# Performance work log

Measured on AMD Instinct MI355X. Metric: run time of the kernel, lower is better.

The kernel has to match this reference:

```python
import jax, jax.numpy as jnp
import numpy as np

DIM = 768
HEADS = 12
DIM_HEAD = 64
INNER = HEADS * DIM_HEAD  # 768
SCALE = DIM_HEAD ** -0.5
LN_EPS = 1e-5


def setup_inputs() -> dict:
    key = jax.random.key(0)
    ks = jax.random.split(key, 6)
    B, N = 2, 1024
    x = jax.random.normal(ks[0], (B, N, DIM), dtype=jnp.float32)
    ln_g = jnp.ones((DIM,), jnp.float32)
    ln_b = jnp.zeros((DIM,), jnp.float32)
    # torch nn.Linear weights are [out, in]
    w_qkv = jax.random.normal(ks[1], (3 * INNER, DIM), jnp.float32) * (DIM ** -0.5)
    w_out = jax.random.normal(ks[2], (DIM, INNER), jnp.float32) * (INNER ** -0.5)
    b_out = jnp.zeros((DIM,), jnp.float32)
    theta = jax.random.normal(ks[3], (HEADS, HEADS), jnp.float32)
    # xavier_uniform for 12x12
    lim = float(np.sqrt(6.0 / (HEADS + HEADS)))
    gnn_w = jax.random.uniform(ks[4], (HEADS, HEADS), jnp.float32, -lim, lim)
    return {"x": x, "ln_g": ln_g, "ln_b": ln_b, "w_qkv": w_qkv,
            "w_out": w_out, "b_out": b_out, "theta": theta, "gnn_w": gnn_w}


def _dc_crd(attn, theta, gnn_w):
    # attn: [B, H, N, N] treated as image with H=12 channels
    B, H, N, _ = attn.shape
    w = attn.mean(axis=(-2, -1))  # adaptive_avg_pool2d -> [B, H]
    diff = w[:, :, None] - w[:, None, :]  # [B, H, H]
    # abs(1 - exp(-d)/(1+exp(-d))) - 1 == abs(1 - sigmoid(-d)) - 1
    T_w = jnp.abs(1.0 - jax.nn.sigmoid(-diff)) - 1.0
    adj = (T_w + jnp.swapaxes(T_w, -1, -2)) * 0.5 * theta  # [B, H, H]
    attn_flat = attn.reshape(B, H, N * N)
    support = jnp.einsum('ij,bjm->bim', gnn_w, attn_flat)  # W @ features
    out = jax.nn.relu(jnp.einsum('bij,bjm->bim', adj, support))  # spmm(adj, support)
    return out.reshape(B, H, N, N)


def reference(x, ln_g, ln_b, w_qkv, w_out, b_out, theta, gnn_w):
    B, N, D = x.shape
    mu = x.mean(-1, keepdims=True)
    var = x.var(-1, keepdims=True)
    xn = (x - mu) * jax.lax.rsqrt(var + LN_EPS) * ln_g + ln_b
    qkv = xn @ w_qkv.T  # [B, N, 3*INNER]
    q, k, v = jnp.split(qkv, 3, axis=-1)
    def heads(t):
        return t.reshape(B, N, HEADS, DIM_HEAD).transpose(0, 2, 1, 3)
    q, k, v = heads(q), heads(k), heads(v)  # [B, H, N, d]
    dots = jnp.einsum('bhnd,bhmd->bhnm', q, k) * SCALE
    attn = jax.nn.softmax(dots, axis=-1)
    H = _dc_crd(attn, theta, gnn_w)
    out = jnp.einsum('bhnm,bhmd->bhnd', attn + H, v)
    out = out.transpose(0, 2, 1, 3).reshape(B, N, INNER)
    return out @ w_out.T + b_out
```

## Files before the change

### kernel.cpp

```cpp
#include <hip/hip_runtime.h>
#include <hip/hip_bf16.h>
#include <stdint.h>

#define NB 2
#define SEQ 1024
#define DMODEL 768
#define NH 12
#define DH 64
#define SCALE 0.125f
#define NCH 4

typedef __hip_bfloat16 bf16;
typedef __attribute__((ext_vector_type(8))) short short8;
typedef __attribute__((ext_vector_type(4))) float f32x4;

__device__ __forceinline__ float b2f(bf16 x){ return __bfloat162float(x); }
__device__ __forceinline__ bf16 f2b(float x){ return __float2bfloat16(x); }
__device__ __forceinline__ short f2bs(float x){
  bf16 h = __float2bfloat16(x); return *reinterpret_cast<short*>(&h);
}
__device__ __forceinline__ float s2f(short u){
  return __uint_as_float(((unsigned)(unsigned short)u) << 16);
}

__global__ __launch_bounds__(256) void cvt_kernel(const float* __restrict__ src,
                                                  bf16* __restrict__ dst, int n){
  int i = blockIdx.x*256 + threadIdx.x;
  if (i < n) dst[i] = f2b(src[i]);
}

__global__ __launch_bounds__(256) void ln_kernel(const float* __restrict__ x,
                                                 const float* __restrict__ g,
                                                 const float* __restrict__ bta,
                                                 bf16* __restrict__ xn){
  int row = blockIdx.x; int t = threadIdx.x;
  const float* xr = x + (size_t)row*DMODEL;
  float v0[3]; float s = 0.f, s2 = 0.f;
  #pragma unroll
  for (int i=0;i<3;i++){ float val = xr[t+256*i]; v0[i]=val; s+=val; s2+=val*val; }
  __shared__ float sb[256], s2b[256];
  sb[t]=s; s2b[t]=s2; __syncthreads();
  for (int off=128; off>0; off>>=1){
    if (t<off){ sb[t]+=sb[t+off]; s2b[t]+=s2b[t+off]; }
    __syncthreads();
  }
  float mean = sb[0]*(1.f/DMODEL);
  float var  = s2b[0]*(1.f/DMODEL) - mean*mean;
  float rstd = rsqrtf(var + 1e-5f);
  #pragma unroll
  for (int i=0;i<3;i++){
    int c = t+256*i;
    xn[(size_t)row*DMODEL + c] = f2b((v0[i]-mean)*rstd*g[c] + bta[c]);
  }
}

__global__ __launch_bounds__(256) void prep_kernel(const float* __restrict__ theta,
                                                   const float* __restrict__ gnn,
                                                   float* __restrict__ Mm,
                                                   float* __restrict__ l){
  int bx = blockIdx.x, t = threadIdx.x;
  if (bx == 0){
    if (t < 144){
      int i = t/12, kx = t%12;
      float sacc = 0.f;
      for (int j=0;j<12;j++) sacc += (-0.5f)*theta[i*12+j] * gnn[j*12+kx];
      Mm[t] = sacc;
    }
  } else {
    l[(bx-1)*256 + t] = 0.f;
  }
}

__global__ __launch_bounds__(256) void gemm_qkv(const bf16* __restrict__ A,
                                                const bf16* __restrict__ W,
                                                bf16* __restrict__ q,
                                                bf16* __restrict__ k,
                                                bf16* __restrict__ vt){
  __shared__ bf16 As[128*32];
  __shared__ bf16 Bs[128*32];
  int n0 = blockIdx.x*128, m0 = blockIdx.y*128;
  int t = threadIdx.x, w = t>>6, lane = t&63;
  int ln16 = lane&15, q8 = (lane>>4)*8;
  int wm = w>>1, wn = w&1;
  f32x4 acc[4][4] = {};
  for (int k0=0; k0<768; k0+=32){
    __syncthreads();
    #pragma unroll
    for (int i=0;i<2;i++){
      int cc = t + i*256;
      int r = cc>>2, ko = (cc&3)*8;
      *(short8*)&As[r*32+ko] = *(const short8*)&A[(size_t)(m0+r)*768 + k0+ko];
      *(short8*)&Bs[r*32+ko] = *(const short8*)&W[(size_t)(n0+r)*768 + k0+ko];
    }
    __syncthreads();
    short8 af[4], bfr[4];
    #pragma unroll
    for (int mi=0;mi<4;mi++) af[mi]  = *(const short8*)&As[(wm*64+mi*16+ln16)*32 + q8];
    #pragma unroll
    for (int ni=0;ni<4;ni++) bfr[ni] = *(const short8*)&Bs[(wn*64+ni*16+ln16)*32 + q8];
    #pragma unroll
    for (int mi=0;mi<4;mi++)
      #pragma unroll
      for (int ni=0;ni<4;ni++)
        acc[mi][ni] = __builtin_amdgcn_mfma_f32_16x16x32_bf16(af[mi], bfr[ni], acc[mi][ni], 0, 0, 0);
  }
  int quad4 = (lane>>4)*4;
  #pragma unroll
  for (int mi=0;mi<4;mi++){
    #pragma unroll
    for (int ni=0;ni<4;ni++){
      int cg = n0 + wn*64 + ni*16 + ln16;
      int which = cg/768; int rem = cg - which*768;
      int h = rem>>6, dd = rem&63;
      #pragma unroll
      for (int r=0;r<4;r++){
        int m = m0 + wm*64 + mi*16 + quad4 + r;
        int bb = m>>10, n = m&1023;
        float val = acc[mi][ni][r];
        if (which==0)      q [((size_t)(bb*NH+h)*SEQ + n)*DH + dd] = f2b(val*SCALE);
        else if (which==1) k [((size_t)(bb*NH+h)*SEQ + n)*DH + dd] = f2b(val);
        else               vt[((size_t)(bb*NH+h)*DH + dd)*SEQ + n] = f2b(val);
      }
    }
  }
}

__global__ __launch_bounds__(768) void attn_sums(const bf16* __restrict__ q,
                                                 const bf16* __restrict__ k,
                                                 float* __restrict__ l){
  int b = blockIdx.z, ch = blockIdx.y; int r0 = blockIdx.x*16;
  int t = threadIdx.x; int h = t>>6; int lane = t&63;
  int ln16 = lane&15, quad = lane>>4; int q8 = quad*8, quad4 = quad*4;
  const bf16* qrow = q + ((size_t)(b*NH+h)*SEQ + r0 + ln16)*DH;
  short8 aq0 = *(const short8*)(qrow + q8);
  short8 aq1 = *(const short8*)(qrow + 32 + q8);
  const bf16* kB = k + ((size_t)(b*NH+h)*SEQ)*DH;
  float ls[4] = {0.f,0.f,0.f,0.f};
  for (int i=0;i<16;i++){
    int c0 = ch*256 + i*16;
    const bf16* krow = kB + (size_t)(c0 + ln16)*DH;
    short8 bk0 = *(const short8*)(krow + q8);
    short8 bk1 = *(const short8*)(krow + 32 + q8);
    f32x4 a = {0.f,0.f,0.f,0.f};
    a = __builtin_amdgcn_mfma_f32_16x16x32_bf16(aq0, bk0, a, 0, 0, 0);
    a = __builtin_amdgcn_mfma_f32_16x16x32_bf16(aq1, bk1, a, 0, 0, 0);
    #pragma unroll
    for (int r=0;r<4;r++) ls[r] += __expf(a[r]);
  }
  #pragma unroll
  for (int msk=1; msk<16; msk<<=1){
    #pragma unroll
    for (int r=0;r<4;r++) ls[r] += __shfl_xor(ls[r], msk);
  }
  if (ln16 == 0){
    #pragma unroll
    for (int r=0;r<4;r++)
      atomicAdd(&l[((size_t)(b*NH+h))*SEQ + r0 + quad4 + r], ls[r]);
  }
}

__global__ __launch_bounds__(768) void attn_main(const bf16* __restrict__ q,
                                                 const bf16* __restrict__ k,
                                                 const bf16* __restrict__ vt,
                                                 const float* __restrict__ Mm,
                                                 const float* __restrict__ l,
                                                 float* __restrict__ opart){
  __shared__ bf16 attT[2][NH][16][40];
  __shared__ float Ms[144];
  int b = blockIdx.z, ch = blockIdx.y; int r0 = blockIdx.x*16;
  int t = threadIdx.x; int h = t>>6; int lane = t&63;
  int ln16 = lane&15, quad = lane>>4; int q8 = quad*8, quad4 = quad*4;
  const bf16* kB = k  + ((size_t)(b*NH+h)*SEQ)*DH;
  const bf16* vB = vt + ((size_t)(b*NH+h)*DH)*SEQ;

  if (t < 144) Ms[t] = Mm[t];

  const bf16* qrow = q + ((size_t)(b*NH+h)*SEQ + r0 + ln16)*DH;
  short8 aq0 = *(const short8*)(qrow + q8);
  short8 aq1 = *(const short8*)(qrow + 32 + q8);

  float inv_l[4];
  #pragma unroll
  for (int r=0;r<4;r++) inv_l[r] = 1.0f / l[((size_t)(b*NH+h))*SEQ + r0 + quad4 + r];

  f32x4 oacc[4] = {};
  for (int it=0; it<8; it++){
    int c0 = ch*256 + it*32;
    int buf = it&1;
    #pragma unroll
    for (int half=0; half<2; half++){
      const bf16* krow = kB + (size_t)(c0 + half*16 + ln16)*DH;
      short8 bk0 = *(const short8*)(krow + q8);
      short8 bk1 = *(const short8*)(krow + 32 + q8);
      f32x4 a = {0.f,0.f,0.f,0.f};
      a = __builtin_amdgcn_mfma_f32_16x16x32_bf16(aq0, bk0, a, 0, 0, 0);
      a = __builtin_amdgcn_mfma_f32_16x16x32_bf16(aq1, bk1, a, 0, 0, 0);
      #pragma unroll
      for (int r=0;r<4;r++)
        attT[buf][h][quad4+r][half*16 + ln16] = f2b(__expf(a[r])*inv_l[r]);
    }
    __syncthreads();
    float sm[8] = {0.f,0.f,0.f,0.f,0.f,0.f,0.f,0.f};
    #pragma unroll
    for (int j=0;j<12;j++){
      short8 u = *(const short8*)&attT[buf][j][ln16][q8];
      float m = Ms[h*12+j];
      #pragma unroll
      for (int e=0;e<8;e++) sm[e] += m*s2f(u[e]);
    }
    short8 uh = *(const short8*)&attT[buf][h][ln16][q8];
    short8 afrag;
    #pragma unroll
    for (int e=0;e<8;e++) afrag[e] = f2bs(s2f(uh[e]) + fmaxf(sm[e], 0.f));
    #pragma unroll
    for (int ni=0; ni<4; ni++){
      short8 bv = *(const short8*)&vB[(size_t)(ni*16 + ln16)*SEQ + c0 + q8];
      oacc[ni] = __builtin_amdgcn_mfma_f32_16x16x32_bf16(afrag, bv, oacc[ni], 0, 0, 0);
    }
  }
  float* dst = opart + ((size_t)ch*NB*SEQ + (size_t)b*SEQ)*DMODEL;
  #pragma unroll
  for (int ni=0; ni<4; ni++)
    #pragma unroll
    for (int r=0; r<4; r++){
      int n = r0 + quad4 + r;
      dst[(size_t)n*DMODEL + h*DH + ni*16 + ln16] = oacc[ni][r];
    }
}

__global__ __launch_bounds__(256) void reduce_kernel(const float* __restrict__ opart,
                                                     bf16* __restrict__ aout){
  const size_t TOT = (size_t)NB*SEQ*DMODEL;
  size_t i = ((size_t)blockIdx.x*256 + threadIdx.x)*4;
  float4 s = *(const float4*)&opart[i];
  #pragma unroll
  for (int c=1;c<NCH;c++){
    float4 p = *(const float4*)&opart[c*TOT + i];
    s.x += p.x; s.y += p.y; s.z += p.z; s.w += p.w;
  }
  aout[i+0]=f2b(s.x); aout[i+1]=f2b(s.y); aout[i+2]=f2b(s.z); aout[i+3]=f2b(s.w);
}

__global__ __launch_bounds__(256) void gemm_out(const bf16* __restrict__ A,
                                                const bf16* __restrict__ W,
                                                const float* __restrict__ bias,
                                                float* __restrict__ out){
  __shared__ bf16 As[128*32];
  __shared__ bf16 Bs[128*32];
  int n0 = blockIdx.x*128, m0 = blockIdx.y*128;
  int t = threadIdx.x, w = t>>6, lane = t&63;
  int ln16 = lane&15, q8 = (lane>>4)*8;
  int wm = w>>1, wn = w&1;
  f32x4 acc[4][4] = {};
  for (int k0=0; k0<768; k0+=32){
    __syncthreads();
    #pragma unroll
    for (int i=0;i<2;i++){
      int cc = t + i*256;
      int r = cc>>2, ko = (cc&3)*8;
      *(short8*)&As[r*32+ko] = *(const short8*)&A[(size_t)(m0+r)*768 + k0+ko];
      *(short8*)&Bs[r*32+ko] = *(const short8*)&W[(size_t)(n0+r)*768 + k0+ko];
    }
    __syncthreads();
    short8 af[4], bfr[4];
    #pragma unroll
    for (int mi=0;mi<4;mi++) af[mi]  = *(const short8*)&As[(wm*64+mi*16+ln16)*32 + q8];
    #pragma unroll
    for (int ni=0;ni<4;ni++) bfr[ni] = *(const short8*)&Bs[(wn*64+ni*16+ln16)*32 + q8];
    #pragma unroll
    for (int mi=0;mi<4;mi++)
      #pragma unroll
      for (int ni=0;ni<4;ni++)
        acc[mi][ni] = __builtin_amdgcn_mfma_f32_16x16x32_bf16(af[mi], bfr[ni], acc[mi][ni], 0, 0, 0);
  }
  int quad4 = (lane>>4)*4;
  #pragma unroll
  for (int mi=0;mi<4;mi++)
    #pragma unroll
    for (int ni=0;ni<4;ni++){
      int cg = n0 + wn*64 + ni*16 + ln16;
      #pragma unroll
      for (int r=0;r<4;r++){
        int m = m0 + wm*64 + mi*16 + quad4 + r;
        out[(size_t)m*768 + cg] = acc[mi][ni][r] + bias[cg];
      }
    }
}

extern "C" void kernel_launch(void* const* d_in, const int* in_sizes, int n_in,
                              void* d_out, int out_size, void* d_ws, size_t ws_size,
                              hipStream_t stream){
  const float* x     = (const float*)d_in[0];
  const float* ln_g  = (const float*)d_in[1];
  const float* ln_b  = (const float*)d_in[2];
  const float* w_qkv = (const float*)d_in[3];
  const float* w_out = (const float*)d_in[4];
  const float* b_out = (const float*)d_in[5];
  const float* theta = (const float*)d_in[6];
  const float* gnn   = (const float*)d_in[7];
  float* out = (float*)d_out;

  char* p = (char*)d_ws;
  bf16* xnb   = (bf16*)p; p += (size_t)2048*768*2;
  bf16* wqkvb = (bf16*)p; p += (size_t)2304*768*2;
  bf16* woutb = (bf16*)p; p += (size_t)768*768*2;
  bf16* qb    = (bf16*)p; p += (size_t)NB*NH*SEQ*DH*2;
  bf16* kb    = (bf16*)p; p += (size_t)NB*NH*SEQ*DH*2;
  bf16* vtb   = (bf16*)p; p += (size_t)NB*NH*SEQ*DH*2;
  bf16* aoutb = (bf16*)p; p += (size_t)2048*768*2;
  float* Mm   = (float*)p; p += 256*4;
  float* lsum = (float*)p; p += (size_t)NB*NH*SEQ*4;
  float* opart= (float*)p;

  cvt_kernel<<<dim3((2304*768+255)/256), dim3(256), 0, stream>>>(w_qkv, wqkvb, 2304*768);
  cvt_kernel<<<dim3((768*768+255)/256),  dim3(256), 0, stream>>>(w_out, woutb, 768*768);
  ln_kernel<<<dim3(NB*SEQ), dim3(256), 0, stream>>>(x, ln_g, ln_b, xnb);
  prep_kernel<<<dim3(97), dim3(256), 0, stream>>>(theta, gnn, Mm, lsum);
  gemm_qkv<<<dim3(18, 16), dim3(256), 0, stream>>>(xnb, wqkvb, qb, kb, vtb);
  attn_sums<<<dim3(64, NCH, NB), dim3(768), 0, stream>>>(qb, kb, lsum);
  attn_main<<<dim3(64, NCH, NB), dim3(768), 0, stream>>>(qb, kb, vtb, Mm, lsum, opart);
  reduce_kernel<<<dim3((NB*SEQ*DMODEL/4+255)/256), dim3(256), 0, stream>>>(opart, aoutb);
  gemm_out<<<dim3(6, 16), dim3(256), 0, stream>>>(aoutb, woutb, b_out, out);
}
```

Baseline: 214.8 us.

## Use direct global-to-LDS loads in GEMMs and fp32 attention staging

Both GEMM kernels now load tiles with the global_load_lds builtin, writing straight into shared memory instead of going through registers. The LDS base per wave is computed as w*64+i*256 times 8, which relies on the hardware placing each lane's 16 bytes consecutively. In attn_main the shared attention tile becomes fp32 (padded to 44), so the 12-head mixing reads float4s and skips bf16 round-tripping, and the V fragment loads are hoisted above the barrier so they overlap with it. attn_sums gets an unroll-4 pragma. The fp32 tile roughly doubles shared-memory use, and the direct-to-LDS addressing is correct only if the builtin's per-lane placement matches the As/Bs layout that readers expect.

Measured after the change: 220.9 us. +2.8%, slower.

```diff
diff --git a/kernel.cpp b/kernel.cpp
--- a/kernel.cpp
+++ b/kernel.cpp
@@ -21,6 +21,12 @@
 }
 __device__ __forceinline__ float s2f(short u){
   return __uint_as_float(((unsigned)(unsigned short)u) << 16);
+}
+
+__device__ __forceinline__ void gl_lds16(const bf16* g, bf16* l){
+  __builtin_amdgcn_global_load_lds(
+      (const __attribute__((address_space(1))) void*)g,
+      (__attribute__((address_space(3))) void*)l, 16, 0, 0);
 }
 
 __global__ __launch_bounds__(256) void cvt_kernel(const float* __restrict__ src,
@@ -89,8 +95,8 @@
     for (int i=0;i<2;i++){
       int cc = t + i*256;
       int r = cc>>2, ko = (cc&3)*8;
-      *(short8*)&As[r*32+ko] = *(const short8*)&A[(size_t)(m0+r)*768 + k0+ko];
-      *(short8*)&Bs[r*32+ko] = *(const short8*)&W[(size_t)(n0+r)*768 + k0+ko];
+      gl_lds16(&A[(size_t)(m0+r)*768 + k0+ko], &As[(size_t)(w*64 + i*256)*8]);
+      gl_lds16(&W[(size_t)(n0+r)*768 + k0+ko], &Bs[(size_t)(w*64 + i*256)*8]);
     }
     __syncthreads();
     short8 af[4], bfr[4];
@@ -136,6 +142,7 @@
   short8 aq1 = *(const short8*)(qrow + 32 + q8);
   const bf16* kB = k + ((size_t)(b*NH+h)*SEQ)*DH;
   float ls[4] = {0.f,0.f,0.f,0.f};
+  #pragma unroll 4
   for (int i=0;i<16;i++){
     int c0 = ch*256 + i*16;
     const bf16* krow = kB + (size_t)(c0 + ln16)*DH;
@@ -165,7 +172,7 @@
                                                  const float* __restrict__ Mm,
                                                  const float* __restrict__ l,
                                                  float* __restrict__ opart){
-  __shared__ bf16 attT[2][NH][16][40];
+  __shared__ float attT[2][NH][16][44];
   __shared__ float Ms[144];
   int b = blockIdx.z, ch = blockIdx.y; int r0 = blockIdx.x*16;
   int t = threadIdx.x; int h = t>>6; int lane = t&63;
@@ -197,26 +204,34 @@
       a = __builtin_amdgcn_mfma_f32_16x16x32_bf16(aq1, bk1, a, 0, 0, 0);
       #pragma unroll
       for (int r=0;r<4;r++)
-        attT[buf][h][quad4+r][half*16 + ln16] = f2b(__expf(a[r])*inv_l[r]);
-    }
+        attT[buf][h][quad4+r][half*16 + ln16] = __expf(a[r])*inv_l[r];
+    }
+    short8 bv[4];
+    #pragma unroll
+    for (int ni=0; ni<4; ni++)
+      bv[ni] = *(const short8*)&vB[(size_t)(ni*16 + ln16)*SEQ + c0 + q8];
     __syncthreads();
     float sm[8] = {0.f,0.f,0.f,0.f,0.f,0.f,0.f,0.f};
     #pragma unroll
     for (int j=0;j<12;j++){
-      short8 u = *(const short8*)&attT[buf][j][ln16][q8];
+      const float* row = &attT[buf][j][ln16][q8];
+      float4 u0 = *(const float4*)row;
+      float4 u1 = *(const float4*)(row+4);
       float m = Ms[h*12+j];
-      #pragma unroll
-      for (int e=0;e<8;e++) sm[e] += m*s2f(u[e]);
-    }
-    short8 uh = *(const short8*)&attT[buf][h][ln16][q8];
+      sm[0] += m*u0.x; sm[1] += m*u0.y; sm[2] += m*u0.z; sm[3] += m*u0.w;
+      sm[4] += m*u1.x; sm[5] += m*u1.y; sm[6] += m*u1.z; sm[7] += m*u1.w;
+    }
+    const float* hrow = &attT[buf][h][ln16][q8];
+    float4 h0 = *(const float4*)hrow;
+    float4 h1 = *(const float4*)(hrow+4);
     short8 afrag;
-    #pragma unroll
-    for (int e=0;e<8;e++) afrag[e] = f2bs(s2f(uh[e]) + fmaxf(sm[e], 0.f));
-    #pragma unroll
-    for (int ni=0; ni<4; ni++){
-      short8 bv = *(const short8*)&vB[(size_t)(ni*16 + ln16)*SEQ + c0 + q8];
-      oacc[ni] = __builtin_amdgcn_mfma_f32_16x16x32_bf16(afrag, bv, oacc[ni], 0, 0, 0);
-    }
+    afrag[0] = f2bs(h0.x + fmaxf(sm[0],0.f)); afrag[1] = f2bs(h0.y + fmaxf(sm[1],0.f));
+    afrag[2] = f2bs(h0.z + fmaxf(sm[2],0.f)); afrag[3] = f2bs(h0.w + fmaxf(sm[3],0.f));
+    afrag[4] = f2bs(h1.x + fmaxf(sm[4],0.f)); afrag[5] = f2bs(h1.y + fmaxf(sm[5],0.f));
+    afrag[6] = f2bs(h1.z + fmaxf(sm[6],0.f)); afrag[7] = f2bs(h1.w + fmaxf(sm[7],0.f));
+    #pragma unroll
+    for (int ni=0; ni<4; ni++)
+      oacc[ni] = __builtin_amdgcn_mfma_f32_16x16x32_bf16(afrag, bv[ni], oacc[ni], 0, 0, 0);
   }
   float* dst = opart + ((size_t)ch*NB*SEQ + (size_t)b*SEQ)*DMODEL;
   #pragma unroll
@@ -258,8 +273,8 @@
     for (int i=0;i<2;i++){
       int cc = t + i*256;
       int r = cc>>2, ko = (cc&3)*8;
-      *(short8*)&As[r*32+ko] = *(const short8*)&A[(size_t)(m0+r)*768 + k0+ko];
-      *(short8*)&Bs[r*32+ko] = *(const short8*)&W[(size_t)(n0+r)*768 + k0+ko];
+      gl_lds16(&A[(size_t)(m0+r)*768 + k0+ko], &As[(size_t)(w*64 + i*256)*8]);
+      gl_lds16(&W[(size_t)(n0+r)*768 + k0+ko], &Bs[(size_t)(w*64 + i*256)*8]);
     }
     __syncthreads();
     short8 af[4], bfr[4];
```

## Materialize exp scores in global memory, fuse prep kernels, use direct LDS loads

Applied to the files above, without the earlier changes.

The prep kernels (layernorm, weight conversion, M matrix and l zeroing) are merged into one launch. attn_exp now writes bf16 exp(QK) values for every head to a 48 MB global buffer alongside the row sums. attn_main reads those values back instead of recomputing QK and exp, folds 1/l into the per-head mixing coefficients, and splits the key dimension into 8 chunks. The GEMMs switch to global_load_lds direct-to-LDS copies. This trades recomputed QK work and LDS staging for heavy extra global memory traffic and a larger partial-sum reduction.

Result: slower. 265.2 us (+23.4%).

```diff
diff --git a/kernel.cpp b/kernel.cpp
--- a/kernel.cpp
+++ b/kernel.cpp
@@ -8,13 +8,13 @@
 #define NH 12
 #define DH 64
 #define SCALE 0.125f
-#define NCH 4
+#define NCHE 4
+#define NCHM 8
 
 typedef __hip_bfloat16 bf16;
 typedef __attribute__((ext_vector_type(8))) short short8;
 typedef __attribute__((ext_vector_type(4))) float f32x4;
 
-__device__ __forceinline__ float b2f(bf16 x){ return __bfloat162float(x); }
 __device__ __forceinline__ bf16 f2b(float x){ return __float2bfloat16(x); }
 __device__ __forceinline__ short f2bs(float x){
   bf16 h = __float2bfloat16(x); return *reinterpret_cast<short*>(&h);
@@ -23,51 +23,59 @@
   return __uint_as_float(((unsigned)(unsigned short)u) << 16);
 }
 
-__global__ __launch_bounds__(256) void cvt_kernel(const float* __restrict__ src,
-                                                  bf16* __restrict__ dst, int n){
-  int i = blockIdx.x*256 + threadIdx.x;
-  if (i < n) dst[i] = f2b(src[i]);
-}
-
-__global__ __launch_bounds__(256) void ln_kernel(const float* __restrict__ x,
-                                                 const float* __restrict__ g,
-                                                 const float* __restrict__ bta,
-                                                 bf16* __restrict__ xn){
-  int row = blockIdx.x; int t = threadIdx.x;
-  const float* xr = x + (size_t)row*DMODEL;
-  float v0[3]; float s = 0.f, s2 = 0.f;
-  #pragma unroll
-  for (int i=0;i<3;i++){ float val = xr[t+256*i]; v0[i]=val; s+=val; s2+=val*val; }
-  __shared__ float sb[256], s2b[256];
-  sb[t]=s; s2b[t]=s2; __syncthreads();
-  for (int off=128; off>0; off>>=1){
-    if (t<off){ sb[t]+=sb[t+off]; s2b[t]+=s2b[t+off]; }
-    __syncthreads();
-  }
-  float mean = sb[0]*(1.f/DMODEL);
-  float var  = s2b[0]*(1.f/DMODEL) - mean*mean;
-  float rstd = rsqrtf(var + 1e-5f);
-  #pragma unroll
-  for (int i=0;i<3;i++){
-    int c = t+256*i;
-    xn[(size_t)row*DMODEL + c] = f2b((v0[i]-mean)*rstd*g[c] + bta[c]);
-  }
-}
-
-__global__ __launch_bounds__(256) void prep_kernel(const float* __restrict__ theta,
-                                                   const float* __restrict__ gnn,
-                                                   float* __restrict__ Mm,
-                                                   float* __restrict__ l){
+__device__ __forceinline__ void gl_lds16(const bf16* g, bf16* l){
+  __builtin_amdgcn_global_load_lds(
+      (const __attribute__((address_space(1))) void*)g,
+      (__attribute__((address_space(3))) void*)l, 16, 0, 0);
+}
+
+__global__ __launch_bounds__(256) void prep_all(const float* __restrict__ x,
+                                                const float* __restrict__ g,
+                                                const float* __restrict__ bta,
+                                                const float* __restrict__ w1, int n1,
+                                                const float* __restrict__ w2, int n2,
+                                                const float* __restrict__ theta,
+                                                const float* __restrict__ gnn,
+                                                bf16* __restrict__ xn,
+                                                bf16* __restrict__ wb,
+                                                float* __restrict__ Mm,
+                                                float* __restrict__ l){
   int bx = blockIdx.x, t = threadIdx.x;
-  if (bx == 0){
-    if (t < 144){
-      int i = t/12, kx = t%12;
-      float sacc = 0.f;
-      for (int j=0;j<12;j++) sacc += (-0.5f)*theta[i*12+j] * gnn[j*12+kx];
-      Mm[t] = sacc;
-    }
+  if (bx < 2048){
+    const float* xr = x + (size_t)bx*DMODEL;
+    float v0[3]; float s = 0.f, s2 = 0.f;
+    #pragma unroll
+    for (int i=0;i<3;i++){ float val = xr[t+256*i]; v0[i]=val; s+=val; s2+=val*val; }
+    __shared__ float sb[256], s2b[256];
+    sb[t]=s; s2b[t]=s2; __syncthreads();
+    for (int off=128; off>0; off>>=1){
+      if (t<off){ sb[t]+=sb[t+off]; s2b[t]+=s2b[t+off]; }
+      __syncthreads();
+    }
+    float mean = sb[0]*(1.f/DMODEL);
+    float var  = s2b[0]*(1.f/DMODEL) - mean*mean;
+    float rstd = rsqrtf(var + 1e-5f);
+    #pragma unroll
+    for (int i=0;i<3;i++){
+      int c = t+256*i;
+      xn[(size_t)bx*DMODEL + c] = f2b((v0[i]-mean)*rstd*g[c] + bta[c]);
+    }
+  } else if (bx < 2048+9216){
+    int i = (bx-2048)*256 + t;
+    if (i < n1) wb[i] = f2b(w1[i]);
+    else if (i < n1+n2) wb[i] = f2b(w2[i-n1]);
   } else {
-    l[(bx-1)*256 + t] = 0.f;
+    int sub = bx - (2048+9216);
+    if (sub == 0){
+      if (t < 144){
+        int i = t/12, kx = t%12;
+        float sacc = 0.f;
+        for (int j=0;j<12;j++) sacc += (-0.5f)*theta[i*12+j] * gnn[j*12+kx];
+        Mm[t] = sacc;
+      }
+    } else {
+      l[(sub-1)*256 + t] = 0.f;
+    }
   }
 }
 
@@ -89,8 +97,8 @@
     for (int i=0;i<2;i++){
       int cc = t + i*256;
       int r = cc>>2, ko = (cc&3)*8;
-      *(short8*)&As[r*32+ko] = *(const short8*)&A[(size_t)(m0+r)*768 + k0+ko];
-      *(short8*)&Bs[r*32+ko] = *(const short8*)&W[(size_t)(n0+r)*768 + k0+ko];
+      gl_lds16(&A[(size_t)(m0+r)*768 + k0+ko], &As[(size_t)(w*64 + i*256)*8]);
+      gl_lds16(&W[(size_t)(n0+r)*768 + k0+ko], &Bs[(size_t)(w*64 + i*256)*8]);
     }
     __syncthreads();
     short8 af[4], bfr[4];
@@ -125,17 +133,22 @@
   }
 }
 
-__global__ __launch_bounds__(768) void attn_sums(const bf16* __restrict__ q,
-                                                 const bf16* __restrict__ k,
-                                                 float* __restrict__ l){
-  int b = blockIdx.z, ch = blockIdx.y; int r0 = blockIdx.x*16;
-  int t = threadIdx.x; int h = t>>6; int lane = t&63;
+__global__ __launch_bounds__(256) void attn_exp(const bf16* __restrict__ q,
+                                                const bf16* __restrict__ k,
+                                                float* __restrict__ l,
+                                                bf16* __restrict__ eg){
+  int strip = blockIdx.x, ch = blockIdx.y;
+  int b = blockIdx.z/3, hg = blockIdx.z%3;
+  int t = threadIdx.x; int h = hg*4 + (t>>6); int lane = t&63;
   int ln16 = lane&15, quad = lane>>4; int q8 = quad*8, quad4 = quad*4;
+  int r0 = strip*16;
   const bf16* qrow = q + ((size_t)(b*NH+h)*SEQ + r0 + ln16)*DH;
   short8 aq0 = *(const short8*)(qrow + q8);
   short8 aq1 = *(const short8*)(qrow + 32 + q8);
   const bf16* kB = k + ((size_t)(b*NH+h)*SEQ)*DH;
+  bf16* egh = eg + (((size_t)(b*NH+h))<<20);
   float ls[4] = {0.f,0.f,0.f,0.f};
+  #pragma unroll 4
   for (int i=0;i<16;i++){
     int c0 = ch*256 + i*16;
     const bf16* krow = kB + (size_t)(c0 + ln16)*DH;
@@ -145,7 +158,11 @@
     a = __builtin_amdgcn_mfma_f32_16x16x32_bf16(aq0, bk0, a, 0, 0, 0);
     a = __builtin_amdgcn_mfma_f32_16x16x32_bf16(aq1, bk1, a, 0, 0, 0);
     #pragma unroll
-    for (int r=0;r<4;r++) ls[r] += __expf(a[r]);
+    for (int r=0;r<4;r++){
+      float e = __expf(a[r]);
+      ls[r] += e;
+      egh[(size_t)(r0+quad4+r)*1024 + c0 + ln16] = f2b(e);
+    }
   }
   #pragma unroll
   for (int msk=1; msk<16; msk<<=1){
@@ -159,59 +176,42 @@
   }
 }
 
-__global__ __launch_bounds__(768) void attn_main(const bf16* __restrict__ q,
-                                                 const bf16* __restrict__ k,
+__global__ __launch_bounds__(768) void attn_main(const bf16* __restrict__ eg,
                                                  const bf16* __restrict__ vt,
                                                  const float* __restrict__ Mm,
                                                  const float* __restrict__ l,
                                                  float* __restrict__ opart){
-  __shared__ bf16 attT[2][NH][16][40];
-  __shared__ float Ms[144];
-  int b = blockIdx.z, ch = blockIdx.y; int r0 = blockIdx.x*16;
+  int strip = blockIdx.x, ch = blockIdx.y, b = blockIdx.z;
   int t = threadIdx.x; int h = t>>6; int lane = t&63;
   int ln16 = lane&15, quad = lane>>4; int q8 = quad*8, quad4 = quad*4;
-  const bf16* kB = k  + ((size_t)(b*NH+h)*SEQ)*DH;
-  const bf16* vB = vt + ((size_t)(b*NH+h)*DH)*SEQ;
-
-  if (t < 144) Ms[t] = Mm[t];
-
-  const bf16* qrow = q + ((size_t)(b*NH+h)*SEQ + r0 + ln16)*DH;
-  short8 aq0 = *(const short8*)(qrow + q8);
-  short8 aq1 = *(const short8*)(qrow + 32 + q8);
-
-  float inv_l[4];
-  #pragma unroll
-  for (int r=0;r<4;r++) inv_l[r] = 1.0f / l[((size_t)(b*NH+h))*SEQ + r0 + quad4 + r];
+  int r0 = strip*16;
+  const bf16* vB  = vt + ((size_t)(b*NH+h)*DH)*SEQ;
+  const bf16* egb = eg + (((size_t)b*NH)<<20);
+  const size_t rowoff = (size_t)(r0 + ln16)*1024;
+
+  float Mp[12];
+  #pragma unroll
+  for (int j=0;j<12;j++){
+    float lj = l[((size_t)(b*NH+j))*SEQ + r0 + ln16];
+    Mp[j] = Mm[h*12+j] / lj;
+  }
+  float ihl = 1.0f / l[((size_t)(b*NH+h))*SEQ + r0 + ln16];
 
   f32x4 oacc[4] = {};
-  for (int it=0; it<8; it++){
-    int c0 = ch*256 + it*32;
-    int buf = it&1;
-    #pragma unroll
-    for (int half=0; half<2; half++){
-      const bf16* krow = kB + (size_t)(c0 + half*16 + ln16)*DH;
-      short8 bk0 = *(const short8*)(krow + q8);
-      short8 bk1 = *(const short8*)(krow + 32 + q8);
-      f32x4 a = {0.f,0.f,0.f,0.f};
-      a = __builtin_amdgcn_mfma_f32_16x16x32_bf16(aq0, bk0, a, 0, 0, 0);
-      a = __builtin_amdgcn_mfma_f32_16x16x32_bf16(aq1, bk1, a, 0, 0, 0);
-      #pragma unroll
-      for (int r=0;r<4;r++)
-        attT[buf][h][quad4+r][half*16 + ln16] = f2b(__expf(a[r])*inv_l[r]);
-    }
-    __syncthreads();
+  for (int it=0; it<4; it++){
+    int c0 = ch*128 + it*32;
     float sm[8] = {0.f,0.f,0.f,0.f,0.f,0.f,0.f,0.f};
     #pragma unroll
     for (int j=0;j<12;j++){
-      short8 u = *(const short8*)&attT[buf][j][ln16][q8];
-      float m = Ms[h*12+j];
+      short8 u = *(const short8*)&egb[(((size_t)j)<<20) + rowoff + c0 + q8];
+      float m = Mp[j];
       #pragma unroll
       for (int e=0;e<8;e++) sm[e] += m*s2f(u[e]);
     }
-    short8 uh = *(const short8*)&attT[buf][h][ln16][q8];
+    short8 uh = *(const short8*)&egb[(((size_t)h)<<20) + rowoff + c0 + q8];
     short8 afrag;
     #pragma unroll
-    for (int e=0;e<8;e++) afrag[e] = f2bs(s2f(uh[e]) + fmaxf(sm[e], 0.f));
+    for (int e=0;e<8;e++) afrag[e] = f2bs(s2f(uh[e])*ihl + fmaxf(sm[e], 0.f));
     #pragma unroll
     for (int ni=0; ni<4; ni++){
       short8 bv = *(const short8*)&vB[(size_t)(ni*16 + ln16)*SEQ + c0 + q8];
@@ -234,7 +234,7 @@
   size_t i = ((size_t)blockIdx.x*256 + threadIdx.x)*4;
   float4 s = *(const float4*)&opart[i];
   #pragma unroll
-  for (int c=1;c<NCH;c++){
+  for (int c=1;c<NCHM;c++){
     float4 p = *(const float4*)&opart[c*TOT + i];
     s.x += p.x; s.y += p.y; s.z += p.z; s.w += p.w;
   }
@@ -258,8 +258,8 @@
     for (int i=0;i<2;i++){
       int cc = t + i*256;
       int r = cc>>2, ko = (cc&3)*8;
-      *(short8*)&As[r*32+ko] = *(const short8*)&A[(size_t)(m0+r)*768 + k0+ko];
-      *(short8*)&Bs[r*32+ko] = *(const short8*)&W[(size_t)(n0+r)*768 + k0+ko];
+      gl_lds16(&A[(size_t)(m0+r)*768 + k0+ko], &As[(size_t)(w*64 + i*256)*8]);
+      gl_lds16(&W[(size_t)(n0+r)*768 + k0+ko], &Bs[(size_t)(w*64 + i*256)*8]);
     }
     __syncthreads();
     short8 af[4], bfr[4];
@@ -310,15 +310,15 @@
   bf16* aoutb = (bf16*)p; p += (size_t)2048*768*2;
   float* Mm   = (float*)p; p += 256*4;
   float* lsum = (float*)p; p += (size_t)NB*NH*SEQ*4;
+  bf16* expg  = (bf16*)p; p += (size_t)NB*NH*SEQ*SEQ*2;
   float* opart= (float*)p;
 
-  cvt_kernel<<<dim3((2304*768+255)/256), dim3(256), 0, stream>>>(w_qkv, wqkvb, 2304*768);
-  cvt_kernel<<<dim3((768*768+255)/256),  dim3(256), 0, stream>>>(w_out, woutb, 768*768);
-  ln_kernel<<<dim3(NB*SEQ), dim3(256), 0, stream>>>(x, ln_g, ln_b, xnb);
-  prep_kernel<<<dim3(97), dim3(256), 0, stream>>>(theta, gnn, Mm, lsum);
+  const int N1 = 2304*768, N2 = 768*768;
+  prep_all<<<dim3(2048+9216+97), dim3(256), 0, stream>>>(
+      x, ln_g, ln_b, w_qkv, N1, w_out, N2, theta, gnn, xnb, wqkvb, Mm, lsum);
   gemm_qkv<<<dim3(18, 16), dim3(256), 0, stream>>>(xnb, wqkvb, qb, kb, vtb);
-  attn_sums<<<dim3(64, NCH, NB), dim3(768), 0, stream>>>(qb, kb, lsum);
-  attn_main<<<dim3(64, NCH, NB), dim3(768), 0, stream>>>(qb, kb, vtb, Mm, lsum, opart);
+  attn_exp<<<dim3(64, NCHE, NB*3), dim3(256), 0, stream>>>(qb, kb, lsum, expg);
+  attn_main<<<dim3(64, NCHM, NB), dim3(768), 0, stream>>>(expg, vtb, Mm, lsum, opart);
   reduce_kernel<<<dim3((NB*SEQ*DMODEL/4+255)/256), dim3(256), 0, stream>>>(opart, aoutb);
   gemm_out<<<dim3(6, 16), dim3(256), 0, stream>>>(aoutb, woutb, b_out, out);
 }
```

## Merge prep kernels, fold chunk reduce into out-GEMM K loop, use global_load_lds

Applied to the files above, without the earlier changes.

Merges LayerNorm, both weight conversions and the theta/gnn prep into one launch. The split-K partial outputs become bf16, and the reduce kernel is removed by having gemm_out run its K loop over all four chunks, which cuts launches and fp32 traffic at the cost of four times the MFMA work in the output GEMM. Both GEMMs now stage tiles with direct global-to-LDS loads, and attn_sums gets an unroll pragma. It risks bf16 rounding of the partial sums, and the LDS destination indexing under global_load_lds has to match the lane layout.

Measured after the change: 246.1 us. 14.6% more time.

```diff
diff --git a/kernel.cpp b/kernel.cpp
--- a/kernel.cpp
+++ b/kernel.cpp
@@ -14,7 +14,6 @@
 typedef __attribute__((ext_vector_type(8))) short short8;
 typedef __attribute__((ext_vector_type(4))) float f32x4;
 
-__device__ __forceinline__ float b2f(bf16 x){ return __bfloat162float(x); }
 __device__ __forceinline__ bf16 f2b(float x){ return __float2bfloat16(x); }
 __device__ __forceinline__ short f2bs(float x){
   bf16 h = __float2bfloat16(x); return *reinterpret_cast<short*>(&h);
@@ -23,51 +22,59 @@
   return __uint_as_float(((unsigned)(unsigned short)u) << 16);
 }
 
-__global__ __launch_bounds__(256) void cvt_kernel(const float* __restrict__ src,
-                                                  bf16* __restrict__ dst, int n){
-  int i = blockIdx.x*256 + threadIdx.x;
-  if (i < n) dst[i] = f2b(src[i]);
-}
-
-__global__ __launch_bounds__(256) void ln_kernel(const float* __restrict__ x,
-                                                 const float* __restrict__ g,
-                                                 const float* __restrict__ bta,
-                                                 bf16* __restrict__ xn){
-  int row = blockIdx.x; int t = threadIdx.x;
-  const float* xr = x + (size_t)row*DMODEL;
-  float v0[3]; float s = 0.f, s2 = 0.f;
-  #pragma unroll
-  for (int i=0;i<3;i++){ float val = xr[t+256*i]; v0[i]=val; s+=val; s2+=val*val; }
-  __shared__ float sb[256], s2b[256];
-  sb[t]=s; s2b[t]=s2; __syncthreads();
-  for (int off=128; off>0; off>>=1){
-    if (t<off){ sb[t]+=sb[t+off]; s2b[t]+=s2b[t+off]; }
-    __syncthreads();
-  }
-  float mean = sb[0]*(1.f/DMODEL);
-  float var  = s2b[0]*(1.f/DMODEL) - mean*mean;
-  float rstd = rsqrtf(var + 1e-5f);
-  #pragma unroll
-  for (int i=0;i<3;i++){
-    int c = t+256*i;
-    xn[(size_t)row*DMODEL + c] = f2b((v0[i]-mean)*rstd*g[c] + bta[c]);
-  }
-}
-
-__global__ __launch_bounds__(256) void prep_kernel(const float* __restrict__ theta,
-                                                   const float* __restrict__ gnn,
-                                                   float* __restrict__ Mm,
-                                                   float* __restrict__ l){
+__device__ __forceinline__ void gl_lds16(const bf16* g, bf16* l){
+  __builtin_amdgcn_global_load_lds(
+      (const __attribute__((address_space(1))) void*)g,
+      (__attribute__((address_space(3))) void*)l, 16, 0, 0);
+}
+
+__global__ __launch_bounds__(256) void prep_all(const float* __restrict__ x,
+                                                const float* __restrict__ g,
+                                                const float* __restrict__ bta,
+                                                const float* __restrict__ w1, int n1,
+                                                const float* __restrict__ w2, int n2,
+                                                const float* __restrict__ theta,
+                                                const float* __restrict__ gnn,
+                                                bf16* __restrict__ xn,
+                                                bf16* __restrict__ wb,
+                                                float* __restrict__ Mm,
+                                                float* __restrict__ l){
   int bx = blockIdx.x, t = threadIdx.x;
-  if (bx == 0){
-    if (t < 144){
-      int i = t/12, kx = t%12;
-      float sacc = 0.f;
-      for (int j=0;j<12;j++) sacc += (-0.5f)*theta[i*12+j] * gnn[j*12+kx];
-      Mm[t] = sacc;
-    }
+  if (bx < 2048){
+    const float* xr = x + (size_t)bx*DMODEL;
+    float v0[3]; float s = 0.f, s2 = 0.f;
+    #pragma unroll
+    for (int i=0;i<3;i++){ float val = xr[t+256*i]; v0[i]=val; s+=val; s2+=val*val; }
+    __shared__ float sb[256], s2b[256];
+    sb[t]=s; s2b[t]=s2; __syncthreads();
+    for (int off=128; off>0; off>>=1){
+      if (t<off){ sb[t]+=sb[t+off]; s2b[t]+=s2b[t+off]; }
+      __syncthreads();
+    }
+    float mean = sb[0]*(1.f/DMODEL);
+    float var  = s2b[0]*(1.f/DMODEL) - mean*mean;
+    float rstd = rsqrtf(var + 1e-5f);
+    #pragma unroll
+    for (int i=0;i<3;i++){
+      int c = t+256*i;
+      xn[(size_t)bx*DMODEL + c] = f2b((v0[i]-mean)*rstd*g[c] + bta[c]);
+    }
+  } else if (bx < 2048+9216){
+    int i = (bx-2048)*256 + t;
+    if (i < n1) wb[i] = f2b(w1[i]);
+    else if (i < n1+n2) wb[i] = f2b(w2[i-n1]);
   } else {
-    l[(bx-1)*256 + t] = 0.f;
+    int sub = bx - (2048+9216);
+    if (sub == 0){
+      if (t < 144){
+        int i = t/12, kx = t%12;
+        float sacc = 0.f;
+        for (int j=0;j<12;j++) sacc += (-0.5f)*theta[i*12+j] * gnn[j*12+kx];
+        Mm[t] = sacc;
+      }
+    } else {
+      l[(sub-1)*256 + t] = 0.f;
+    }
   }
 }
 
@@ -89,8 +96,8 @@
     for (int i=0;i<2;i++){
       int cc = t + i*256;
       int r = cc>>2, ko = (cc&3)*8;
-      *(short8*)&As[r*32+ko] = *(const short8*)&A[(size_t)(m0+r)*768 + k0+ko];
-      *(short8*)&Bs[r*32+ko] = *(const short8*)&W[(size_t)(n0+r)*768 + k0+ko];
+      gl_lds16(&A[(size_t)(m0+r)*768 + k0+ko], &As[(size_t)(w*64 + i*256)*8]);
+      gl_lds16(&W[(size_t)(n0+r)*768 + k0+ko], &Bs[(size_t)(w*64 + i*256)*8]);
     }
     __syncthreads();
     short8 af[4], bfr[4];
@@ -136,6 +143,7 @@
   short8 aq1 = *(const short8*)(qrow + 32 + q8);
   const bf16* kB = k + ((size_t)(b*NH+h)*SEQ)*DH;
   float ls[4] = {0.f,0.f,0.f,0.f};
+  #pragma unroll 4
   for (int i=0;i<16;i++){
     int c0 = ch*256 + i*16;
     const bf16* krow = kB + (size_t)(c0 + ln16)*DH;
@@ -164,7 +172,7 @@
                                                  const bf16* __restrict__ vt,
                                                  const float* __restrict__ Mm,
                                                  const float* __restrict__ l,
-                                                 float* __restrict__ opart){
+                                                 bf16* __restrict__ opart){
   __shared__ bf16 attT[2][NH][16][40];
   __shared__ float Ms[144];
   int b = blockIdx.z, ch = blockIdx.y; int r0 = blockIdx.x*16;
@@ -218,30 +226,17 @@
       oacc[ni] = __builtin_amdgcn_mfma_f32_16x16x32_bf16(afrag, bv, oacc[ni], 0, 0, 0);
     }
   }
-  float* dst = opart + ((size_t)ch*NB*SEQ + (size_t)b*SEQ)*DMODEL;
+  bf16* dst = opart + ((size_t)ch*NB*SEQ + (size_t)b*SEQ)*DMODEL;
   #pragma unroll
   for (int ni=0; ni<4; ni++)
     #pragma unroll
     for (int r=0; r<4; r++){
       int n = r0 + quad4 + r;
-      dst[(size_t)n*DMODEL + h*DH + ni*16 + ln16] = oacc[ni][r];
-    }
-}
-
-__global__ __launch_bounds__(256) void reduce_kernel(const float* __restrict__ opart,
-                                                     bf16* __restrict__ aout){
-  const size_t TOT = (size_t)NB*SEQ*DMODEL;
-  size_t i = ((size_t)blockIdx.x*256 + threadIdx.x)*4;
-  float4 s = *(const float4*)&opart[i];
-  #pragma unroll
-  for (int c=1;c<NCH;c++){
-    float4 p = *(const float4*)&opart[c*TOT + i];
-    s.x += p.x; s.y += p.y; s.z += p.z; s.w += p.w;
-  }
-  aout[i+0]=f2b(s.x); aout[i+1]=f2b(s.y); aout[i+2]=f2b(s.z); aout[i+3]=f2b(s.w);
-}
-
-__global__ __launch_bounds__(256) void gemm_out(const bf16* __restrict__ A,
+      dst[(size_t)n*DMODEL + h*DH + ni*16 + ln16] = f2b(oacc[ni][r]);
+    }
+}
+
+__global__ __launch_bounds__(256) void gemm_out(const bf16* __restrict__ opart,
                                                 const bf16* __restrict__ W,
                                                 const float* __restrict__ bias,
                                                 float* __restrict__ out){
@@ -252,14 +247,16 @@
   int ln16 = lane&15, q8 = (lane>>4)*8;
   int wm = w>>1, wn = w&1;
   f32x4 acc[4][4] = {};
-  for (int k0=0; k0<768; k0+=32){
+  for (int k0=0; k0<NCH*768; k0+=32){
+    int ch = k0/768, kk0 = k0 - ch*768;
+    const bf16* Aب = opart + (size_t)ch*NB*SEQ*DMODEL;
     __syncthreads();
     #pragma unroll
     for (int i=0;i<2;i++){
       int cc = t + i*256;
       int r = cc>>2, ko = (cc&3)*8;
-      *(short8*)&As[r*32+ko] = *(const short8*)&A[(size_t)(m0+r)*768 + k0+ko];
-      *(short8*)&Bs[r*32+ko] = *(const short8*)&W[(size_t)(n0+r)*768 + k0+ko];
+      gl_lds16(&Aب[(size_t)(m0+r)*768 + kk0+ko], &As[(size_t)(w*64 + i*256)*8]);
+      gl_lds16(&W[(size_t)(n0+r)*768 + kk0+ko], &Bs[(size_t)(w*64 + i*256)*8]);
     }
     __syncthreads();
     short8 af[4], bfr[4];
@@ -307,18 +304,15 @@
   bf16* qb    = (bf16*)p; p += (size_t)NB*NH*SEQ*DH*2;
   bf16* kb    = (bf16*)p; p += (size_t)NB*NH*SEQ*DH*2;
   bf16* vtb   = (bf16*)p; p += (size_t)NB*NH*SEQ*DH*2;
-  bf16* aoutb = (bf16*)p; p += (size_t)2048*768*2;
   float* Mm   = (float*)p; p += 256*4;
   float* lsum = (float*)p; p += (size_t)NB*NH*SEQ*4;
-  float* opart= (float*)p;
-
-  cvt_kernel<<<dim3((2304*768+255)/256), dim3(256), 0, stream>>>(w_qkv, wqkvb, 2304*768);
-  cvt_kernel<<<dim3((768*768+255)/256),  dim3(256), 0, stream>>>(w_out, woutb, 768*768);
-  ln_kernel<<<dim3(NB*SEQ), dim3(256), 0, stream>>>(x, ln_g, ln_b, xnb);
-  prep_kernel<<<dim3(97), dim3(256), 0, stream>>>(theta, gnn, Mm, lsum);
+  bf16* opart = (bf16*)p;
+
+  const int N1 = 2304*768, N2 = 768*768;
+  prep_all<<<dim3(2048+9216+97), dim3(256), 0, stream>>>(
+      x, ln_g, ln_b, w_qkv, N1, w_out, N2, theta, gnn, xnb, wqkvb, Mm, lsum);
   gemm_qkv<<<dim3(18, 16), dim3(256), 0, stream>>>(xnb, wqkvb, qb, kb, vtb);
   attn_sums<<<dim3(64, NCH, NB), dim3(768), 0, stream>>>(qb, kb, lsum);
   attn_main<<<dim3(64, NCH, NB), dim3(768), 0, stream>>>(qb, kb, vtb, Mm, lsum, opart);
-  reduce_kernel<<<dim3((NB*SEQ*DMODEL/4+255)/256), dim3(256), 0, stream>>>(opart, aoutb);
-  gemm_out<<<dim3(6, 16), dim3(256), 0, stream>>>(aoutb, woutb, b_out, out);
-}
+  gemm_out<<<dim3(6, 16), dim3(256), 0, stream>>>(opart, woutb, b_out, out);
+}
```
